# Kernel tuning notes

Hardware: AMD Instinct MI355X
Metric: run time of the kernel (lower is better)

Reference implementation:

```python
import jax, jax.numpy as jnp
import numpy as np

B, N, U = 8, 4096, 128
AVG_DEG = 32.0  # expected neighbors per node


def setup_inputs() -> dict:
    key = jax.random.key(0)
    k1, k2, k3 = jax.random.split(key, 3)
    x = jax.random.normal(k1, (B, N, U), dtype=jnp.float32)
    # sparse-ish binary adjacency, ~AVG_DEG neighbors per node
    adj = (jax.random.uniform(k2, (B, N, N)) < (AVG_DEG / N)).astype(jnp.float32)
    W = jax.random.normal(k3, (U, U), dtype=jnp.float32) * 0.05
    b = jnp.zeros((U,), dtype=jnp.float32)
    return {"x": x, "adj": adj, "W": W, "b": b}


def reference(x, adj, W, b):
    # adjacency is stop_gradient'd in the original module
    adj = jax.lax.stop_gradient(adj)

    def step(h):
        # batched SpMM (dense here): [B,N,N] @ [B,N,U] -> [B,N,U]
        hn = jnp.einsum('bij,bjd->bid', adj, h)
        # aggregate_mode='graph_conv': no degree normalization
        return jax.nn.swish(hn @ W + b)

    # eval mode: K_l = 2 message-passing iterations
    return step(step(x))
```

## Files before the change

kernel.cpp:

```cpp
#include <hip/hip_runtime.h>
#include <math.h>

#define BB 8
#define NN 4096
#define UU 128
#define CAP 128

typedef float f4_t __attribute__((ext_vector_type(4)));

__global__ __launch_bounds__(256) void build_idx_kernel(
    const float* __restrict__ adj,
    unsigned short* __restrict__ idx,
    int* __restrict__ deg)
{
    const int row = blockIdx.x;
    const f4_t* arow = (const f4_t*)(adj + (size_t)row * NN);

    __shared__ int cnt;
    __shared__ unsigned short sidx[CAP];
    if (threadIdx.x == 0) cnt = 0;
    __syncthreads();

    #pragma unroll
    for (int it = 0; it < 4; ++it) {
        const int v = it * 256 + threadIdx.x;
        const f4_t a = __builtin_nontemporal_load(arow + v);
        const int jb = v * 4;
        if (a[0] != 0.f) { int p = atomicAdd(&cnt, 1); if (p < CAP) sidx[p] = (unsigned short)(jb + 0); }
        if (a[1] != 0.f) { int p = atomicAdd(&cnt, 1); if (p < CAP) sidx[p] = (unsigned short)(jb + 1); }
        if (a[2] != 0.f) { int p = atomicAdd(&cnt, 1); if (p < CAP) sidx[p] = (unsigned short)(jb + 2); }
        if (a[3] != 0.f) { int p = atomicAdd(&cnt, 1); if (p < CAP) sidx[p] = (unsigned short)(jb + 3); }
    }
    __syncthreads();

    int d = cnt; if (d > CAP) d = CAP;
    if (threadIdx.x == 0) deg[row] = d;
    for (int t = (int)threadIdx.x; t < d; t += 256)
        idx[(size_t)row * CAP + t] = sidx[t];
}

__global__ __launch_bounds__(256) void aggregate_kernel(
    const float* __restrict__ h,
    const unsigned short* __restrict__ idx,
    const int* __restrict__ deg,
    float* __restrict__ hn)
{
    __shared__ unsigned short sidx[8 * CAP];
    __shared__ int sdeg[8];

    const int row0 = blockIdx.x * 8;

    {
        const uint4* g = (const uint4*)(idx + (size_t)row0 * CAP);
        if (threadIdx.x < 128) ((uint4*)sidx)[threadIdx.x] = g[threadIdx.x];
        if (threadIdx.x < 8)   sdeg[threadIdx.x] = deg[row0 + threadIdx.x];
    }
    __syncthreads();

    const int rg   = threadIdx.x >> 5;
    const int lane = threadIdx.x & 31;
    const int row  = row0 + rg;
    const int b    = row >> 12;

    const float4* hb = (const float4*)(h + (size_t)b * NN * UU);
    const unsigned short* my = &sidx[rg * CAP];
    const int d = sdeg[rg];

    float4 a0 = make_float4(0.f,0.f,0.f,0.f), a1 = a0, a2 = a0, a3 = a0;
    int n = 0;
    for (; n + 8 <= d; n += 8) {
        const int j0 = my[n+0], j1 = my[n+1], j2 = my[n+2], j3 = my[n+3];
        const int j4 = my[n+4], j5 = my[n+5], j6 = my[n+6], j7 = my[n+7];
        const float4 v0 = hb[j0 * 32 + lane];
        const float4 v1 = hb[j1 * 32 + lane];
        const float4 v2 = hb[j2 * 32 + lane];
        const float4 v3 = hb[j3 * 32 + lane];
        const float4 v4 = hb[j4 * 32 + lane];
        const float4 v5 = hb[j5 * 32 + lane];
        const float4 v6 = hb[j6 * 32 + lane];
        const float4 v7 = hb[j7 * 32 + lane];
        a0.x += v0.x + v4.x; a0.y += v0.y + v4.y; a0.z += v0.z + v4.z; a0.w += v0.w + v4.w;
        a1.x += v1.x + v5.x; a1.y += v1.y + v5.y; a1.z += v1.z + v5.z; a1.w += v1.w + v5.w;
        a2.x += v2.x + v6.x; a2.y += v2.y + v6.y; a2.z += v2.z + v6.z; a2.w += v2.w + v6.w;
        a3.x += v3.x + v7.x; a3.y += v3.y + v7.y; a3.z += v3.z + v7.z; a3.w += v3.w + v7.w;
    }
    for (; n < d; ++n) {
        const int j = my[n];
        const float4 v = hb[j * 32 + lane];
        a0.x += v.x; a0.y += v.y; a0.z += v.z; a0.w += v.w;
    }
    float4 acc;
    acc.x = (a0.x + a1.x) + (a2.x + a3.x);
    acc.y = (a0.y + a1.y) + (a2.y + a3.y);
    acc.z = (a0.z + a1.z) + (a2.z + a3.z);
    acc.w = (a0.w + a1.w) + (a2.w + a3.w);
    ((float4*)hn)[(size_t)row * 32 + lane] = acc;
}

__global__ __launch_bounds__(256) void gemm_swish_kernel(
    const float* __restrict__ hn,
    const float* __restrict__ Wm,
    const float* __restrict__ bias,
    float* __restrict__ out)
{
    __shared__ float s[64 * UU];

    const int row0 = blockIdx.x * 64;
    const float4* src = (const float4*)(hn + (size_t)row0 * UU);
    float4* d4 = (float4*)s;
    #pragma unroll
    for (int i = 0; i < 8; ++i)
        d4[i * 256 + threadIdx.x] = src[i * 256 + threadIdx.x];
    __syncthreads();

    const int cg = threadIdx.x & 31;
    const int r0 = (threadIdx.x >> 5) * 8;

    float acc[8][4];
    #pragma unroll
    for (int r = 0; r < 8; ++r)
        #pragma unroll
        for (int c = 0; c < 4; ++c) acc[r][c] = 0.f;

    const float4* W4 = (const float4*)Wm;
    #pragma unroll 4
    for (int k = 0; k < UU; k += 4) {
        const float4 w0 = W4[(k + 0) * 32 + cg];
        const float4 w1 = W4[(k + 1) * 32 + cg];
        const float4 w2 = W4[(k + 2) * 32 + cg];
        const float4 w3 = W4[(k + 3) * 32 + cg];
        #pragma unroll
        for (int r = 0; r < 8; ++r) {
            const float4 sv = *(const float4*)&s[(r0 + r) * UU + k];
            acc[r][0] += sv.x * w0.x + sv.y * w1.x + sv.z * w2.x + sv.w * w3.x;
            acc[r][1] += sv.x * w0.y + sv.y * w1.y + sv.z * w2.y + sv.w * w3.y;
            acc[r][2] += sv.x * w0.z + sv.y * w1.z + sv.z * w2.z + sv.w * w3.z;
            acc[r][3] += sv.x * w0.w + sv.y * w1.w + sv.z * w2.w + sv.w * w3.w;
        }
    }

    const float4 bb = ((const float4*)bias)[cg];
    #pragma unroll
    for (int r = 0; r < 8; ++r) {
        const int row = row0 + r0 + r;
        float4 o;
        float v;
        v = acc[r][0] + bb.x; o.x = v / (1.f + expf(-v));
        v = acc[r][1] + bb.y; o.y = v / (1.f + expf(-v));
        v = acc[r][2] + bb.z; o.z = v / (1.f + expf(-v));
        v = acc[r][3] + bb.w; o.w = v / (1.f + expf(-v));
        ((float4*)out)[(size_t)row * 32 + cg] = o;
    }
}

extern "C" void kernel_launch(void* const* d_in, const int* in_sizes, int n_in,
                              void* d_out, int out_size, void* d_ws, size_t ws_size,
                              hipStream_t stream)
{
    const float* x    = (const float*)d_in[0];
    const float* adj  = (const float*)d_in[1];
    const float* Wm   = (const float*)d_in[2];
    const float* bias = (const float*)d_in[3];
    float* out = (float*)d_out;

    const int R = BB * NN;

    char* ws = (char*)d_ws;
    unsigned short* idx = (unsigned short*)ws;
    int* deg = (int*)(ws + (size_t)R * CAP * sizeof(unsigned short));
    float* hn = (float*)(ws + (size_t)R * CAP * sizeof(unsigned short)
                            + (size_t)R * sizeof(int));

    build_idx_kernel<<<R, 256, 0, stream>>>(adj, idx, deg);

    aggregate_kernel<<<R / 8, 256, 0, stream>>>(x, idx, deg, hn);
    gemm_swish_kernel<<<R / 64, 256, 0, stream>>>(hn, Wm, bias, out);

    aggregate_kernel<<<R / 8, 256, 0, stream>>>(out, idx, deg, hn);
    gemm_swish_kernel<<<R / 64, 256, 0, stream>>>(hn, Wm, bias, out);
}
```

Measured before the change: 784.0 us.

## Fuse index build, neighbor gather and GEMM+swish into two per-hop kernels

Replaces the five-kernel pipeline (index build, two aggregate passes, two GEMM+swish passes) with two kernels. The first builds the neighbor index for 8 rows per block, gathers from x and applies W plus swish. The second gathers from h1 and applies the GEMM. This drops the hn intermediate round-trips through global memory and three launches. The tail loop is replaced by a padded, masked 8-wide gather. The trade-off is that the GEMM now reuses W across only 8 rows per block instead of 64, so W traffic from cache rises and the matmul becomes less efficient.

```diff
diff --git a/kernel.cpp b/kernel.cpp
--- a/kernel.cpp
+++ b/kernel.cpp
@@ -5,68 +5,31 @@
 #define NN 4096
 #define UU 128
 #define CAP 128
+#define RPB 8
 
 typedef float f4_t __attribute__((ext_vector_type(4)));
 
-__global__ __launch_bounds__(256) void build_idx_kernel(
-    const float* __restrict__ adj,
-    unsigned short* __restrict__ idx,
-    int* __restrict__ deg)
+__device__ __forceinline__ void gather_gemm_swish(
+    const unsigned short* __restrict__ sidx,
+    const int* __restrict__ sdeg,
+    float (*shn)[UU],
+    const float* __restrict__ hsrc,
+    const float* __restrict__ Wm,
+    const float* __restrict__ bias,
+    float* __restrict__ dst,
+    int row0)
 {
-    const int row = blockIdx.x;
-    const f4_t* arow = (const f4_t*)(adj + (size_t)row * NN);
-
-    __shared__ int cnt;
-    __shared__ unsigned short sidx[CAP];
-    if (threadIdx.x == 0) cnt = 0;
-    __syncthreads();
-
-    #pragma unroll
-    for (int it = 0; it < 4; ++it) {
-        const int v = it * 256 + threadIdx.x;
-        const f4_t a = __builtin_nontemporal_load(arow + v);
-        const int jb = v * 4;
-        if (a[0] != 0.f) { int p = atomicAdd(&cnt, 1); if (p < CAP) sidx[p] = (unsigned short)(jb + 0); }
-        if (a[1] != 0.f) { int p = atomicAdd(&cnt, 1); if (p < CAP) sidx[p] = (unsigned short)(jb + 1); }
-        if (a[2] != 0.f) { int p = atomicAdd(&cnt, 1); if (p < CAP) sidx[p] = (unsigned short)(jb + 2); }
-        if (a[3] != 0.f) { int p = atomicAdd(&cnt, 1); if (p < CAP) sidx[p] = (unsigned short)(jb + 3); }
-    }
-    __syncthreads();
-
-    int d = cnt; if (d > CAP) d = CAP;
-    if (threadIdx.x == 0) deg[row] = d;
-    for (int t = (int)threadIdx.x; t < d; t += 256)
-        idx[(size_t)row * CAP + t] = sidx[t];
-}
-
-__global__ __launch_bounds__(256) void aggregate_kernel(
-    const float* __restrict__ h,
-    const unsigned short* __restrict__ idx,
-    const int* __restrict__ deg,
-    float* __restrict__ hn)
-{
-    __shared__ unsigned short sidx[8 * CAP];
-    __shared__ int sdeg[8];
-
-    const int row0 = blockIdx.x * 8;
-
-    {
-        const uint4* g = (const uint4*)(idx + (size_t)row0 * CAP);
-        if (threadIdx.x < 128) ((uint4*)sidx)[threadIdx.x] = g[threadIdx.x];
-        if (threadIdx.x < 8)   sdeg[threadIdx.x] = deg[row0 + threadIdx.x];
-    }
-    __syncthreads();
-
     const int rg   = threadIdx.x >> 5;
     const int lane = threadIdx.x & 31;
     const int row  = row0 + rg;
     const int b    = row >> 12;
 
-    const float4* hb = (const float4*)(h + (size_t)b * NN * UU);
+    const float4* hb = (const float4*)(hsrc + (size_t)b * NN * UU);
     const unsigned short* my = &sidx[rg * CAP];
     const int d = sdeg[rg];
 
     float4 a0 = make_float4(0.f,0.f,0.f,0.f), a1 = a0, a2 = a0, a3 = a0;
+
     int n = 0;
     for (; n + 8 <= d; n += 8) {
         const int j0 = my[n+0], j1 = my[n+1], j2 = my[n+2], j3 = my[n+3];
@@ -84,73 +47,123 @@
         a2.x += v2.x + v6.x; a2.y += v2.y + v6.y; a2.z += v2.z + v6.z; a2.w += v2.w + v6.w;
         a3.x += v3.x + v7.x; a3.y += v3.y + v7.y; a3.z += v3.z + v7.z; a3.w += v3.w + v7.w;
     }
-    for (; n < d; ++n) {
-        const int j = my[n];
-        const float4 v = hb[j * 32 + lane];
-        a0.x += v.x; a0.y += v.y; a0.z += v.z; a0.w += v.w;
+    if (n < d) {
+        const int j0 = my[n+0], j1 = my[n+1], j2 = my[n+2], j3 = my[n+3];
+        const int j4 = my[n+4], j5 = my[n+5], j6 = my[n+6], j7 = my[n+7];
+        const float4 v0 = hb[j0 * 32 + lane];
+        const float4 v1 = hb[j1 * 32 + lane];
+        const float4 v2 = hb[j2 * 32 + lane];
+        const float4 v3 = hb[j3 * 32 + lane];
+        const float4 v4 = hb[j4 * 32 + lane];
+        const float4 v5 = hb[j5 * 32 + lane];
+        const float4 v6 = hb[j6 * 32 + lane];
+        const float4 v7 = hb[j7 * 32 + lane];
+        const float m0 = (n+0 < d) ? 1.f : 0.f, m1 = (n+1 < d) ? 1.f : 0.f;
+        const float m2 = (n+2 < d) ? 1.f : 0.f, m3 = (n+3 < d) ? 1.f : 0.f;
+        const float m4 = (n+4 < d) ? 1.f : 0.f, m5 = (n+5 < d) ? 1.f : 0.f;
+        const float m6 = (n+6 < d) ? 1.f : 0.f, m7 = (n+7 < d) ? 1.f : 0.f;
+        a0.x += v0.x*m0 + v4.x*m4; a0.y += v0.y*m0 + v4.y*m4; a0.z += v0.z*m0 + v4.z*m4; a0.w += v0.w*m0 + v4.w*m4;
+        a1.x += v1.x*m1 + v5.x*m5; a1.y += v1.y*m1 + v5.y*m5; a1.z += v1.z*m1 + v5.z*m5; a1.w += v1.w*m1 + v5.w*m5;
+        a2.x += v2.x*m2 + v6.x*m6; a2.y += v2.y*m2 + v6.y*m6; a2.z += v2.z*m2 + v6.z*m6; a2.w += v2.w*m2 + v6.w*m6;
+        a3.x += v3.x*m3 + v7.x*m7; a3.y += v3.y*m3 + v7.y*m7; a3.z += v3.z*m3 + v7.z*m7; a3.w += v3.w*m3 + v7.w*m7;
     }
+
     float4 acc;
     acc.x = (a0.x + a1.x) + (a2.x + a3.x);
     acc.y = (a0.y + a1.y) + (a2.y + a3.y);
     acc.z = (a0.z + a1.z) + (a2.z + a3.z);
     acc.w = (a0.w + a1.w) + (a2.w + a3.w);
-    ((float4*)hn)[(size_t)row * 32 + lane] = acc;
+    ((float4*)shn[rg])[lane] = acc;
+    __syncthreads();
+
+    float ac0 = 0.f, ac1 = 0.f, ac2 = 0.f, ac3 = 0.f;
+    const float4* W4 = (const float4*)Wm;
+    const float* hr = shn[rg];
+    #pragma unroll 4
+    for (int k = 0; k < UU; k += 4) {
+        const float4 w0 = W4[(k + 0) * 32 + lane];
+        const float4 w1 = W4[(k + 1) * 32 + lane];
+        const float4 w2 = W4[(k + 2) * 32 + lane];
+        const float4 w3 = W4[(k + 3) * 32 + lane];
+        const float4 sv = *(const float4*)&hr[k];
+        ac0 += sv.x * w0.x + sv.y * w1.x + sv.z * w2.x + sv.w * w3.x;
+        ac1 += sv.x * w0.y + sv.y * w1.y + sv.z * w2.y + sv.w * w3.y;
+        ac2 += sv.x * w0.z + sv.y * w1.z + sv.z * w2.z + sv.w * w3.z;
+        ac3 += sv.x * w0.w + sv.y * w1.w + sv.z * w2.w + sv.w * w3.w;
+    }
+    const float4 bb4 = ((const float4*)bias)[lane];
+    float4 o; float v;
+    v = ac0 + bb4.x; o.x = v / (1.f + expf(-v));
+    v = ac1 + bb4.y; o.y = v / (1.f + expf(-v));
+    v = ac2 + bb4.z; o.z = v / (1.f + expf(-v));
+    v = ac3 + bb4.w; o.w = v / (1.f + expf(-v));
+    ((float4*)dst)[(size_t)row * 32 + lane] = o;
 }
 
-__global__ __launch_bounds__(256) void gemm_swish_kernel(
-    const float* __restrict__ hn,
+__global__ __launch_bounds__(256) void hop1_kernel(
+    const float* __restrict__ x,
+    const float* __restrict__ adj,
+    const float* __restrict__ Wm,
+    const float* __restrict__ bias,
+    unsigned short* __restrict__ idx,
+    int* __restrict__ deg,
+    float* __restrict__ h1)
+{
+    __shared__ unsigned short sidx[RPB * CAP];
+    __shared__ int scnt[RPB];
+    __shared__ float shn[RPB][UU];
+
+    const int row0 = blockIdx.x * RPB;
+    if (threadIdx.x < RPB) scnt[threadIdx.x] = 0;
+    __syncthreads();
+
+    const f4_t* ab = (const f4_t*)(adj + (size_t)row0 * NN);
+    #pragma unroll 8
+    for (int i = 0; i < 32; ++i) {
+        const int g  = i * 256 + (int)threadIdx.x;
+        const f4_t a = __builtin_nontemporal_load(ab + g);
+        const int rr = g >> 10;
+        const int jb = (g & 1023) * 4;
+        if (a[0] != 0.f) { int p = atomicAdd(&scnt[rr], 1); if (p < CAP) sidx[rr*CAP + p] = (unsigned short)(jb + 0); }
+        if (a[1] != 0.f) { int p = atomicAdd(&scnt[rr], 1); if (p < CAP) sidx[rr*CAP + p] = (unsigned short)(jb + 1); }
+        if (a[2] != 0.f) { int p = atomicAdd(&scnt[rr], 1); if (p < CAP) sidx[rr*CAP + p] = (unsigned short)(jb + 2); }
+        if (a[3] != 0.f) { int p = atomicAdd(&scnt[rr], 1); if (p < CAP) sidx[rr*CAP + p] = (unsigned short)(jb + 3); }
+    }
+    __syncthreads();
+
+    const int rg   = threadIdx.x >> 5;
+    const int lane = threadIdx.x & 31;
+    const int row  = row0 + rg;
+    int d = scnt[rg]; if (d > CAP) d = CAP;
+    const int dpad = (d + 7) & ~7;
+    for (int t = d + lane; t < dpad; t += 32) sidx[rg*CAP + t] = 0;
+    if (lane == 0) { scnt[rg] = d; deg[row] = d; }
+    for (int t = lane; t < dpad; t += 32)
+        idx[(size_t)row * CAP + t] = sidx[rg*CAP + t];
+    __syncthreads();
+
+    gather_gemm_swish(sidx, scnt, shn, x, Wm, bias, h1, row0);
+}
+
+__global__ __launch_bounds__(256) void hop2_kernel(
+    const float* __restrict__ h1,
+    const unsigned short* __restrict__ idx,
+    const int* __restrict__ deg,
     const float* __restrict__ Wm,
     const float* __restrict__ bias,
     float* __restrict__ out)
 {
-    __shared__ float s[64 * UU];
+    __shared__ unsigned short sidx[RPB * CAP];
+    __shared__ int sdeg[RPB];
+    __shared__ float shn[RPB][UU];
 
-    const int row0 = blockIdx.x * 64;
-    const float4* src = (const float4*)(hn + (size_t)row0 * UU);
-    float4* d4 = (float4*)s;
-    #pragma unroll
-    for (int i = 0; i < 8; ++i)
-        d4[i * 256 + threadIdx.x] = src[i * 256 + threadIdx.x];
+    const int row0 = blockIdx.x * RPB;
+    const uint4* g = (const uint4*)(idx + (size_t)row0 * CAP);
+    if (threadIdx.x < 128) ((uint4*)sidx)[threadIdx.x] = g[threadIdx.x];
+    if (threadIdx.x < RPB) sdeg[threadIdx.x] = deg[row0 + threadIdx.x];
     __syncthreads();
 
-    const int cg = threadIdx.x & 31;
-    const int r0 = (threadIdx.x >> 5) * 8;
-
-    float acc[8][4];
-    #pragma unroll
-    for (int r = 0; r < 8; ++r)
-        #pragma unroll
-        for (int c = 0; c < 4; ++c) acc[r][c] = 0.f;
-
-    const float4* W4 = (const float4*)Wm;
-    #pragma unroll 4
-    for (int k = 0; k < UU; k += 4) {
-        const float4 w0 = W4[(k + 0) * 32 + cg];
-        const float4 w1 = W4[(k + 1) * 32 + cg];
-        const float4 w2 = W4[(k + 2) * 32 + cg];
-        const float4 w3 = W4[(k + 3) * 32 + cg];
-        #pragma unroll
-        for (int r = 0; r < 8; ++r) {
-            const float4 sv = *(const float4*)&s[(r0 + r) * UU + k];
-            acc[r][0] += sv.x * w0.x + sv.y * w1.x + sv.z * w2.x + sv.w * w3.x;
-            acc[r][1] += sv.x * w0.y + sv.y * w1.y + sv.z * w2.y + sv.w * w3.y;
-            acc[r][2] += sv.x * w0.z + sv.y * w1.z + sv.z * w2.z + sv.w * w3.z;
-            acc[r][3] += sv.x * w0.w + sv.y * w1.w + sv.z * w2.w + sv.w * w3.w;
-        }
-    }
-
-    const float4 bb = ((const float4*)bias)[cg];
-    #pragma unroll
-    for (int r = 0; r < 8; ++r) {
-        const int row = row0 + r0 + r;
-        float4 o;
-        float v;
-        v = acc[r][0] + bb.x; o.x = v / (1.f + expf(-v));
-        v = acc[r][1] + bb.y; o.y = v / (1.f + expf(-v));
-        v = acc[r][2] + bb.z; o.z = v / (1.f + expf(-v));
-        v = acc[r][3] + bb.w; o.w = v / (1.f + expf(-v));
-        ((float4*)out)[(size_t)row * 32 + cg] = o;
-    }
+    gather_gemm_swish(sidx, sdeg, shn, h1, Wm, bias, out, row0);
 }
 
 extern "C" void kernel_launch(void* const* d_in, const int* in_sizes, int n_in,
@@ -168,14 +181,9 @@
     char* ws = (char*)d_ws;
     unsigned short* idx = (unsigned short*)ws;
     int* deg = (int*)(ws + (size_t)R * CAP * sizeof(unsigned short));
-    float* hn = (float*)(ws + (size_t)R * CAP * sizeof(unsigned short)
-                            + (size_t)R * sizeof(int));
+    float* h1 = (float*)(ws + (size_t)R * CAP * sizeof(unsigned short)
+                             + (size_t)R * sizeof(int));
 
-    build_idx_kernel<<<R, 256, 0, stream>>>(adj, idx, deg);
-
-    aggregate_kernel<<<R / 8, 256, 0, stream>>>(x, idx, deg, hn);
-    gemm_swish_kernel<<<R / 64, 256, 0, stream>>>(hn, Wm, bias, out);
-
-    aggregate_kernel<<<R / 8, 256, 0, stream>>>(out, idx, deg, hn);
-    gemm_swish_kernel<<<R / 64, 256, 0, stream>>>(hn, Wm, bias, out);
+    hop1_kernel<<<R / RPB, 256, 0, stream>>>(x, adj, Wm, bias, idx, deg, h1);
+    hop2_kernel<<<R / RPB, 256, 0, stream>>>(h1, idx, deg, Wm, bias, out);
 }
```

Result: slower. 825.6 us (+5.3%).

## Remap block IDs per XCD so each batch stays in one L2, pad neighbor tails

Applied to the files above, without the earlier changes.

Block indices in all three kernels are remapped so that consecutive hardware block IDs, which are dispatched round-robin across the 8 XCDs, map to rows of the same batch. Each XCD's L2 then holds one batch's features during the gather. The neighbor lists are zero-padded to a multiple of 8 so the scalar tail loop can become a masked 8-wide unrolled gather. Index loads use nontemporal hints, and the intermediate activation moves to a separate workspace buffer. The cost is some redundant masked loads of row 0 in the tail.

```diff
diff --git a/kernel.cpp b/kernel.cpp
--- a/kernel.cpp
+++ b/kernel.cpp
@@ -5,15 +5,20 @@
 #define NN 4096
 #define UU 128
 #define CAP 128
+#define RPB 8
+#define NXCD 8
 
 typedef float f4_t __attribute__((ext_vector_type(4)));
+typedef unsigned int u4_t __attribute__((ext_vector_type(4)));
 
 __global__ __launch_bounds__(256) void build_idx_kernel(
     const float* __restrict__ adj,
     unsigned short* __restrict__ idx,
     int* __restrict__ deg)
 {
-    const int row = blockIdx.x;
+    const int bid = blockIdx.x;
+    const int row = (bid & (NXCD - 1)) * NN + (bid >> 3);
+
     const f4_t* arow = (const f4_t*)(adj + (size_t)row * NN);
 
     __shared__ int cnt;
@@ -34,8 +39,11 @@
     __syncthreads();
 
     int d = cnt; if (d > CAP) d = CAP;
+    const int dpad = (d + 7) & ~7;
+    for (int t = d + (int)threadIdx.x; t < dpad; t += 256) sidx[t] = 0;
     if (threadIdx.x == 0) deg[row] = d;
-    for (int t = (int)threadIdx.x; t < d; t += 256)
+    __syncthreads();
+    for (int t = (int)threadIdx.x; t < dpad; t += 256)
         idx[(size_t)row * CAP + t] = sidx[t];
 }
 
@@ -45,15 +53,18 @@
     const int* __restrict__ deg,
     float* __restrict__ hn)
 {
-    __shared__ unsigned short sidx[8 * CAP];
-    __shared__ int sdeg[8];
-
-    const int row0 = blockIdx.x * 8;
+    __shared__ unsigned short sidx[RPB * CAP];
+    __shared__ int sdeg[RPB];
+
+    const int bid  = blockIdx.x;
+    const int rb   = (bid & (NXCD - 1)) * (BB * NN / RPB / NXCD) + (bid >> 3);
+    const int row0 = rb * RPB;
 
     {
-        const uint4* g = (const uint4*)(idx + (size_t)row0 * CAP);
-        if (threadIdx.x < 128) ((uint4*)sidx)[threadIdx.x] = g[threadIdx.x];
-        if (threadIdx.x < 8)   sdeg[threadIdx.x] = deg[row0 + threadIdx.x];
+        const u4_t* g = (const u4_t*)(idx + (size_t)row0 * CAP);
+        if (threadIdx.x < 128)
+            ((u4_t*)sidx)[threadIdx.x] = __builtin_nontemporal_load(g + threadIdx.x);
+        if (threadIdx.x < RPB) sdeg[threadIdx.x] = deg[row0 + threadIdx.x];
     }
     __syncthreads();
 
@@ -67,6 +78,7 @@
     const int d = sdeg[rg];
 
     float4 a0 = make_float4(0.f,0.f,0.f,0.f), a1 = a0, a2 = a0, a3 = a0;
+
     int n = 0;
     for (; n + 8 <= d; n += 8) {
         const int j0 = my[n+0], j1 = my[n+1], j2 = my[n+2], j3 = my[n+3];
@@ -84,11 +96,27 @@
         a2.x += v2.x + v6.x; a2.y += v2.y + v6.y; a2.z += v2.z + v6.z; a2.w += v2.w + v6.w;
         a3.x += v3.x + v7.x; a3.y += v3.y + v7.y; a3.z += v3.z + v7.z; a3.w += v3.w + v7.w;
     }
-    for (; n < d; ++n) {
-        const int j = my[n];
-        const float4 v = hb[j * 32 + lane];
-        a0.x += v.x; a0.y += v.y; a0.z += v.z; a0.w += v.w;
-    }
+    if (n < d) {
+        const int j0 = my[n+0], j1 = my[n+1], j2 = my[n+2], j3 = my[n+3];
+        const int j4 = my[n+4], j5 = my[n+5], j6 = my[n+6], j7 = my[n+7];
+        const float4 v0 = hb[j0 * 32 + lane];
+        const float4 v1 = hb[j1 * 32 + lane];
+        const float4 v2 = hb[j2 * 32 + lane];
+        const float4 v3 = hb[j3 * 32 + lane];
+        const float4 v4 = hb[j4 * 32 + lane];
+        const float4 v5 = hb[j5 * 32 + lane];
+        const float4 v6 = hb[j6 * 32 + lane];
+        const float4 v7 = hb[j7 * 32 + lane];
+        const float m0 = (n+0 < d) ? 1.f : 0.f, m1 = (n+1 < d) ? 1.f : 0.f;
+        const float m2 = (n+2 < d) ? 1.f : 0.f, m3 = (n+3 < d) ? 1.f : 0.f;
+        const float m4 = (n+4 < d) ? 1.f : 0.f, m5 = (n+5 < d) ? 1.f : 0.f;
+        const float m6 = (n+6 < d) ? 1.f : 0.f, m7 = (n+7 < d) ? 1.f : 0.f;
+        a0.x += v0.x*m0 + v4.x*m4; a0.y += v0.y*m0 + v4.y*m4; a0.z += v0.z*m0 + v4.z*m4; a0.w += v0.w*m0 + v4.w*m4;
+        a1.x += v1.x*m1 + v5.x*m5; a1.y += v1.y*m1 + v5.y*m5; a1.z += v1.z*m1 + v5.z*m5; a1.w += v1.w*m1 + v5.w*m5;
+        a2.x += v2.x*m2 + v6.x*m6; a2.y += v2.y*m2 + v6.y*m6; a2.z += v2.z*m2 + v6.z*m6; a2.w += v2.w*m2 + v6.w*m6;
+        a3.x += v3.x*m3 + v7.x*m7; a3.y += v3.y*m3 + v7.y*m7; a3.z += v3.z*m3 + v7.z*m7; a3.w += v3.w*m3 + v7.w*m7;
+    }
+
     float4 acc;
     acc.x = (a0.x + a1.x) + (a2.x + a3.x);
     acc.y = (a0.y + a1.y) + (a2.y + a3.y);
@@ -105,7 +133,10 @@
 {
     __shared__ float s[64 * UU];
 
-    const int row0 = blockIdx.x * 64;
+    const int bid  = blockIdx.x;
+    const int rbb  = (bid & (NXCD - 1)) * (512 / NXCD) + (bid >> 3);
+    const int row0 = rbb * 64;
+
     const float4* src = (const float4*)(hn + (size_t)row0 * UU);
     float4* d4 = (float4*)s;
     #pragma unroll
@@ -139,16 +170,16 @@
         }
     }
 
-    const float4 bb = ((const float4*)bias)[cg];
+    const float4 bb4 = ((const float4*)bias)[cg];
     #pragma unroll
     for (int r = 0; r < 8; ++r) {
         const int row = row0 + r0 + r;
         float4 o;
         float v;
-        v = acc[r][0] + bb.x; o.x = v / (1.f + expf(-v));
-        v = acc[r][1] + bb.y; o.y = v / (1.f + expf(-v));
-        v = acc[r][2] + bb.z; o.z = v / (1.f + expf(-v));
-        v = acc[r][3] + bb.w; o.w = v / (1.f + expf(-v));
+        v = acc[r][0] + bb4.x; o.x = v / (1.f + expf(-v));
+        v = acc[r][1] + bb4.y; o.y = v / (1.f + expf(-v));
+        v = acc[r][2] + bb4.z; o.z = v / (1.f + expf(-v));
+        v = acc[r][3] + bb4.w; o.w = v / (1.f + expf(-v));
         ((float4*)out)[(size_t)row * 32 + cg] = o;
     }
 }
@@ -169,13 +200,14 @@
     unsigned short* idx = (unsigned short*)ws;
     int* deg = (int*)(ws + (size_t)R * CAP * sizeof(unsigned short));
     float* hn = (float*)(ws + (size_t)R * CAP * sizeof(unsigned short)
-                            + (size_t)R * sizeof(int));
+                             + (size_t)R * sizeof(int));
+    float* h1 = hn + (size_t)R * UU;
 
     build_idx_kernel<<<R, 256, 0, stream>>>(adj, idx, deg);
 
-    aggregate_kernel<<<R / 8, 256, 0, stream>>>(x, idx, deg, hn);
-    gemm_swish_kernel<<<R / 64, 256, 0, stream>>>(hn, Wm, bias, out);
-
-    aggregate_kernel<<<R / 8, 256, 0, stream>>>(out, idx, deg, hn);
-    gemm_swish_kernel<<<R / 64, 256, 0, stream>>>(hn, Wm, bias, out);
-}
+    aggregate_kernel<<<R / RPB, 256, 0, stream>>>(x, idx, deg, hn);
+    gemm_swish_kernel<<<512, 256, 0, stream>>>(hn, Wm, bias, h1);
+
+    aggregate_kernel<<<R / RPB, 256, 0, stream>>>(h1, idx, deg, hn);
+    gemm_swish_kernel<<<512, 256, 0, stream>>>(hn, Wm, bias, out);
+}
```

After: 795.0 us. No clear change (+1.4%).

## Replace sparse gather aggregation with dense bf16 MFMA adjacency GEMM fused with swish

Applied to the files above, without the earlier changes.

Drops the neighbor-index build and the gather-based aggregation. Each hop now computes adj @ h as a dense GEMM on bf16 MFMA, with 128-row tiles and register-prefetched K chunks. The W matmul, bias and swish are fused into the same kernel epilogue through LDS. Inputs are converted to bf16 first, and the first hop writes bf16 output for the second hop. This trades the atomic-heavy index build and the separate passes for reading the dense adjacency twice, and it lowers the precision of h to bf16.

```diff
diff --git a/kernel.cpp b/kernel.cpp
--- a/kernel.cpp
+++ b/kernel.cpp
@@ -4,152 +4,194 @@
 #define BB 8
 #define NN 4096
 #define UU 128
-#define CAP 128
-
-typedef float f4_t __attribute__((ext_vector_type(4)));
-
-__global__ __launch_bounds__(256) void build_idx_kernel(
+#define BM 128
+#define BK 64
+#define NXCD 8
+
+typedef float  f4_t   __attribute__((ext_vector_type(4)));
+typedef float  f32x4  __attribute__((ext_vector_type(4)));
+typedef unsigned int u32x4 __attribute__((ext_vector_type(4)));
+typedef unsigned int u32x2 __attribute__((ext_vector_type(2)));
+typedef short  bf16x8 __attribute__((ext_vector_type(8)));
+
+static __device__ __forceinline__ unsigned int pack2_trunc(float lo, float hi) {
+    return (__float_as_uint(hi) & 0xFFFF0000u) | (__float_as_uint(lo) >> 16);
+}
+static __device__ __forceinline__ unsigned int bf16_rne1(float f) {
+    unsigned int u = __float_as_uint(f);
+    return (u + 0x7FFFu + ((u >> 16) & 1u)) >> 16;
+}
+static __device__ __forceinline__ unsigned int pack2_rne(float lo, float hi) {
+    return bf16_rne1(lo) | (bf16_rne1(hi) << 16);
+}
+
+__global__ __launch_bounds__(256) void cvt_bf16_kernel(
+    const float* __restrict__ in, unsigned short* __restrict__ outb)
+{
+    const size_t i = ((size_t)blockIdx.x * 256 + threadIdx.x) * 8;
+    const f4_t v0 = *(const f4_t*)(in + i);
+    const f4_t v1 = *(const f4_t*)(in + i + 4);
+    u32x4 o;
+    o.x = pack2_rne(v0[0], v0[1]);
+    o.y = pack2_rne(v0[2], v0[3]);
+    o.z = pack2_rne(v1[0], v1[1]);
+    o.w = pack2_rne(v1[2], v1[3]);
+    *(u32x4*)(outb + i) = o;
+}
+
+template<int OUT_BF16>
+__global__ __launch_bounds__(512) void hop_kernel(
     const float* __restrict__ adj,
-    unsigned short* __restrict__ idx,
-    int* __restrict__ deg)
-{
-    const int row = blockIdx.x;
-    const f4_t* arow = (const f4_t*)(adj + (size_t)row * NN);
-
-    __shared__ int cnt;
-    __shared__ unsigned short sidx[CAP];
-    if (threadIdx.x == 0) cnt = 0;
-    __syncthreads();
-
-    #pragma unroll
-    for (int it = 0; it < 4; ++it) {
-        const int v = it * 256 + threadIdx.x;
-        const f4_t a = __builtin_nontemporal_load(arow + v);
-        const int jb = v * 4;
-        if (a[0] != 0.f) { int p = atomicAdd(&cnt, 1); if (p < CAP) sidx[p] = (unsigned short)(jb + 0); }
-        if (a[1] != 0.f) { int p = atomicAdd(&cnt, 1); if (p < CAP) sidx[p] = (unsigned short)(jb + 1); }
-        if (a[2] != 0.f) { int p = atomicAdd(&cnt, 1); if (p < CAP) sidx[p] = (unsigned short)(jb + 2); }
-        if (a[3] != 0.f) { int p = atomicAdd(&cnt, 1); if (p < CAP) sidx[p] = (unsigned short)(jb + 3); }
-    }
-    __syncthreads();
-
-    int d = cnt; if (d > CAP) d = CAP;
-    if (threadIdx.x == 0) deg[row] = d;
-    for (int t = (int)threadIdx.x; t < d; t += 256)
-        idx[(size_t)row * CAP + t] = sidx[t];
-}
-
-__global__ __launch_bounds__(256) void aggregate_kernel(
-    const float* __restrict__ h,
-    const unsigned short* __restrict__ idx,
-    const int* __restrict__ deg,
-    float* __restrict__ hn)
-{
-    __shared__ unsigned short sidx[8 * CAP];
-    __shared__ int sdeg[8];
-
-    const int row0 = blockIdx.x * 8;
-
-    {
-        const uint4* g = (const uint4*)(idx + (size_t)row0 * CAP);
-        if (threadIdx.x < 128) ((uint4*)sidx)[threadIdx.x] = g[threadIdx.x];
-        if (threadIdx.x < 8)   sdeg[threadIdx.x] = deg[row0 + threadIdx.x];
-    }
-    __syncthreads();
-
-    const int rg   = threadIdx.x >> 5;
-    const int lane = threadIdx.x & 31;
-    const int row  = row0 + rg;
-    const int b    = row >> 12;
-
-    const float4* hb = (const float4*)(h + (size_t)b * NN * UU);
-    const unsigned short* my = &sidx[rg * CAP];
-    const int d = sdeg[rg];
-
-    float4 a0 = make_float4(0.f,0.f,0.f,0.f), a1 = a0, a2 = a0, a3 = a0;
-    int n = 0;
-    for (; n + 8 <= d; n += 8) {
-        const int j0 = my[n+0], j1 = my[n+1], j2 = my[n+2], j3 = my[n+3];
-        const int j4 = my[n+4], j5 = my[n+5], j6 = my[n+6], j7 = my[n+7];
-        const float4 v0 = hb[j0 * 32 + lane];
-        const float4 v1 = hb[j1 * 32 + lane];
-        const float4 v2 = hb[j2 * 32 + lane];
-        const float4 v3 = hb[j3 * 32 + lane];
-        const float4 v4 = hb[j4 * 32 + lane];
-        const float4 v5 = hb[j5 * 32 + lane];
-        const float4 v6 = hb[j6 * 32 + lane];
-        const float4 v7 = hb[j7 * 32 + lane];
-        a0.x += v0.x + v4.x; a0.y += v0.y + v4.y; a0.z += v0.z + v4.z; a0.w += v0.w + v4.w;
-        a1.x += v1.x + v5.x; a1.y += v1.y + v5.y; a1.z += v1.z + v5.z; a1.w += v1.w + v5.w;
-        a2.x += v2.x + v6.x; a2.y += v2.y + v6.y; a2.z += v2.z + v6.z; a2.w += v2.w + v6.w;
-        a3.x += v3.x + v7.x; a3.y += v3.y + v7.y; a3.z += v3.z + v7.z; a3.w += v3.w + v7.w;
-    }
-    for (; n < d; ++n) {
-        const int j = my[n];
-        const float4 v = hb[j * 32 + lane];
-        a0.x += v.x; a0.y += v.y; a0.z += v.z; a0.w += v.w;
-    }
-    float4 acc;
-    acc.x = (a0.x + a1.x) + (a2.x + a3.x);
-    acc.y = (a0.y + a1.y) + (a2.y + a3.y);
-    acc.z = (a0.z + a1.z) + (a2.z + a3.z);
-    acc.w = (a0.w + a1.w) + (a2.w + a3.w);
-    ((float4*)hn)[(size_t)row * 32 + lane] = acc;
-}
-
-__global__ __launch_bounds__(256) void gemm_swish_kernel(
-    const float* __restrict__ hn,
+    const unsigned short* __restrict__ hsrc,
     const float* __restrict__ Wm,
     const float* __restrict__ bias,
-    float* __restrict__ out)
+    void* __restrict__ dst)
 {
-    __shared__ float s[64 * UU];
-
-    const int row0 = blockIdx.x * 64;
-    const float4* src = (const float4*)(hn + (size_t)row0 * UU);
-    float4* d4 = (float4*)s;
-    #pragma unroll
-    for (int i = 0; i < 8; ++i)
-        d4[i * 256 + threadIdx.x] = src[i * 256 + threadIdx.x];
+    __shared__ __align__(16) char smem[128 * 132 * 4];
+    short* sA  = (short*)smem;
+    short* sH  = sA + 128 * 72;
+    float* sHN = (float*)smem;
+
+    const int t  = threadIdx.x;
+    const int b  = blockIdx.x & (NXCD - 1);
+    const int i0 = (blockIdx.x >> 3) * BM;
+
+    const float* ab          = adj  + (size_t)b * NN * NN;
+    const unsigned short* hb = hsrc + (size_t)b * NN * UU;
+
+    const int ar = t >> 2, aq = t & 3;
+    const int sa_off = ar * 72 + aq * 16;
+    const int hk = t & 63, hc0 = (t >> 6) * 16;
+
+    const int wid = t >> 6, lane = t & 63;
+    const int wm = wid >> 2;
+    const int wn = wid & 3;
+    const int fr = lane & 15, fq = lane >> 4;
+
+    f32x4 acc[4][2];
+    #pragma unroll
+    for (int m = 0; m < 4; ++m)
+        #pragma unroll
+        for (int n = 0; n < 2; ++n)
+            acc[m][n] = (f32x4){0.f, 0.f, 0.f, 0.f};
+
+    int aoff[4], boff[2];
+    #pragma unroll
+    for (int m = 0; m < 4; ++m) aoff[m] = (wm * 64 + m * 16 + fr) * 72 + fq * 8;
+    #pragma unroll
+    for (int n = 0; n < 2; ++n) boff[n] = (wn * 32 + n * 16 + fr) * 72 + fq * 8;
+
+    f4_t  areg[4];
+    u32x4 hreg0, hreg1;
+
+    auto LOAD = [&](int k0) {
+        const f4_t* ap = (const f4_t*)(ab + (size_t)(i0 + ar) * NN + k0) + aq * 4;
+        areg[0] = __builtin_nontemporal_load(ap + 0);
+        areg[1] = __builtin_nontemporal_load(ap + 1);
+        areg[2] = __builtin_nontemporal_load(ap + 2);
+        areg[3] = __builtin_nontemporal_load(ap + 3);
+        const u32x4* hp = (const u32x4*)(hb + (size_t)(k0 + hk) * UU + hc0);
+        hreg0 = hp[0];
+        hreg1 = hp[1];
+    };
+
+    auto STORE_LDS = [&]() {
+        u32x4 lo, hi;
+        lo.x = pack2_trunc(areg[0][0], areg[0][1]);
+        lo.y = pack2_trunc(areg[0][2], areg[0][3]);
+        lo.z = pack2_trunc(areg[1][0], areg[1][1]);
+        lo.w = pack2_trunc(areg[1][2], areg[1][3]);
+        hi.x = pack2_trunc(areg[2][0], areg[2][1]);
+        hi.y = pack2_trunc(areg[2][2], areg[2][3]);
+        hi.z = pack2_trunc(areg[3][0], areg[3][1]);
+        hi.w = pack2_trunc(areg[3][2], areg[3][3]);
+        *(u32x4*)&sA[sa_off]     = lo;
+        *(u32x4*)&sA[sa_off + 8] = hi;
+        unsigned short hv[16];
+        *(u32x4*)&hv[0] = hreg0;
+        *(u32x4*)&hv[8] = hreg1;
+        #pragma unroll
+        for (int j = 0; j < 16; ++j)
+            sH[(hc0 + j) * 72 + hk] = (short)hv[j];
+    };
+
+    LOAD(0);
+    #pragma unroll 1
+    for (int c = 0; c < NN / BK; ++c) {
+        STORE_LDS();
+        __syncthreads();
+        if (c < NN / BK - 1) LOAD((c + 1) * BK);
+        #pragma unroll
+        for (int ks = 0; ks < 2; ++ks) {
+            bf16x8 av[4], bv[2];
+            const int kb = ks * 32;
+            #pragma unroll
+            for (int m = 0; m < 4; ++m) av[m] = *(const bf16x8*)&sA[aoff[m] + kb];
+            #pragma unroll
+            for (int n = 0; n < 2; ++n) bv[n] = *(const bf16x8*)&sH[boff[n] + kb];
+            #pragma unroll
+            for (int m = 0; m < 4; ++m)
+                #pragma unroll
+                for (int n = 0; n < 2; ++n)
+                    acc[m][n] = __builtin_amdgcn_mfma_f32_16x16x32_bf16(
+                        av[m], bv[n], acc[m][n], 0, 0, 0);
+        }
+        __syncthreads();
+    }
+
+    #pragma unroll
+    for (int m = 0; m < 4; ++m)
+        #pragma unroll
+        for (int n = 0; n < 2; ++n)
+            #pragma unroll
+            for (int r = 0; r < 4; ++r)
+                sHN[(wm * 64 + m * 16 + fq * 4 + r) * 132
+                    + (wn * 32 + n * 16 + fr)] = acc[m][n][r];
     __syncthreads();
 
-    const int cg = threadIdx.x & 31;
-    const int r0 = (threadIdx.x >> 5) * 8;
-
-    float acc[8][4];
+    const int cg = t & 31;
+    const int r0 = (t >> 5) * 8;
+    float aw[8][4];
     #pragma unroll
     for (int r = 0; r < 8; ++r)
         #pragma unroll
-        for (int c = 0; c < 4; ++c) acc[r][c] = 0.f;
-
-    const float4* W4 = (const float4*)Wm;
+        for (int cxx = 0; cxx < 4; ++cxx) aw[r][cxx] = 0.f;
+
+    const f4_t* W4 = (const f4_t*)Wm;
     #pragma unroll 4
     for (int k = 0; k < UU; k += 4) {
-        const float4 w0 = W4[(k + 0) * 32 + cg];
-        const float4 w1 = W4[(k + 1) * 32 + cg];
-        const float4 w2 = W4[(k + 2) * 32 + cg];
-        const float4 w3 = W4[(k + 3) * 32 + cg];
+        const f4_t w0 = W4[(k + 0) * 32 + cg];
+        const f4_t w1 = W4[(k + 1) * 32 + cg];
+        const f4_t w2 = W4[(k + 2) * 32 + cg];
+        const f4_t w3 = W4[(k + 3) * 32 + cg];
         #pragma unroll
         for (int r = 0; r < 8; ++r) {
-            const float4 sv = *(const float4*)&s[(r0 + r) * UU + k];
-            acc[r][0] += sv.x * w0.x + sv.y * w1.x + sv.z * w2.x + sv.w * w3.x;
-            acc[r][1] += sv.x * w0.y + sv.y * w1.y + sv.z * w2.y + sv.w * w3.y;
-            acc[r][2] += sv.x * w0.z + sv.y * w1.z + sv.z * w2.z + sv.w * w3.z;
-            acc[r][3] += sv.x * w0.w + sv.y * w1.w + sv.z * w2.w + sv.w * w3.w;
+            const f4_t sv = *(const f4_t*)&sHN[(r0 + r) * 132 + k];
+            aw[r][0] += sv[0]*w0[0] + sv[1]*w1[0] + sv[2]*w2[0] + sv[3]*w3[0];
+            aw[r][1] += sv[0]*w0[1] + sv[1]*w1[1] + sv[2]*w2[1] + sv[3]*w3[1];
+            aw[r][2] += sv[0]*w0[2] + sv[1]*w1[2] + sv[2]*w2[2] + sv[3]*w3[2];
+            aw[r][3] += sv[0]*w0[3] + sv[1]*w1[3] + sv[2]*w2[3] + sv[3]*w3[3];
         }
     }
 
-    const float4 bb = ((const float4*)bias)[cg];
+    const f4_t bb4 = ((const f4_t*)bias)[cg];
     #pragma unroll
     for (int r = 0; r < 8; ++r) {
-        const int row = row0 + r0 + r;
-        float4 o;
-        float v;
-        v = acc[r][0] + bb.x; o.x = v / (1.f + expf(-v));
-        v = acc[r][1] + bb.y; o.y = v / (1.f + expf(-v));
-        v = acc[r][2] + bb.z; o.z = v / (1.f + expf(-v));
-        v = acc[r][3] + bb.w; o.w = v / (1.f + expf(-v));
-        ((float4*)out)[(size_t)row * 32 + cg] = o;
+        const size_t row = (size_t)b * NN + i0 + r0 + r;
+        float v, o0, o1, o2, o3;
+        v = aw[r][0] + bb4[0]; o0 = v / (1.f + expf(-v));
+        v = aw[r][1] + bb4[1]; o1 = v / (1.f + expf(-v));
+        v = aw[r][2] + bb4[2]; o2 = v / (1.f + expf(-v));
+        v = aw[r][3] + bb4[3]; o3 = v / (1.f + expf(-v));
+        if (OUT_BF16) {
+            u32x2 p;
+            p.x = pack2_rne(o0, o1);
+            p.y = pack2_rne(o2, o3);
+            *(u32x2*)((unsigned short*)dst + row * UU + cg * 4) = p;
+        } else {
+            f4_t o = {o0, o1, o2, o3};
+            *(f4_t*)((float*)dst + row * UU + cg * 4) = o;
+        }
     }
 }
 
@@ -163,19 +205,12 @@
     const float* bias = (const float*)d_in[3];
     float* out = (float*)d_out;
 
-    const int R = BB * NN;
-
-    char* ws = (char*)d_ws;
-    unsigned short* idx = (unsigned short*)ws;
-    int* deg = (int*)(ws + (size_t)R * CAP * sizeof(unsigned short));
-    float* hn = (float*)(ws + (size_t)R * CAP * sizeof(unsigned short)
-                            + (size_t)R * sizeof(int));
-
-    build_idx_kernel<<<R, 256, 0, stream>>>(adj, idx, deg);
-
-    aggregate_kernel<<<R / 8, 256, 0, stream>>>(x, idx, deg, hn);
-    gemm_swish_kernel<<<R / 64, 256, 0, stream>>>(hn, Wm, bias, out);
-
-    aggregate_kernel<<<R / 8, 256, 0, stream>>>(out, idx, deg, hn);
-    gemm_swish_kernel<<<R / 64, 256, 0, stream>>>(hn, Wm, bias, out);
-}
+    unsigned short* xb  = (unsigned short*)d_ws;
+    unsigned short* h1b = xb + (size_t)BB * NN * UU;
+
+    cvt_bf16_kernel<<<(BB * NN * UU) / (256 * 8), 256, 0, stream>>>(x, xb);
+
+    hop_kernel<1><<<BB * (NN / BM), 512, 0, stream>>>(adj, xb, Wm, bias, (void*)h1b);
+
+    hop_kernel<0><<<BB * (NN / BM), 512, 0, stream>>>(adj, h1b, Wm, bias, (void*)out);
+}
```

Result: slower. 1.013 ms (+29.1%).
